# Kernel optimization log

Hardware: AMD Instinct MI355X
Metric: run time of the kernel (lower is better)

Reference implementation:

```python
import jax, jax.numpy as jnp
import numpy as np

NEG_SLOPE = 0.2  # PyG GATConv default


def gat_conv(x, src, dst, W, a_src, a_dst, bias, n):
    # x: [N, Fin] -> h: [N, Fout]
    h = x @ W
    alpha_s = h @ a_src  # [N]
    alpha_d = h @ a_dst  # [N]
    e = jax.nn.leaky_relu(alpha_s[src] + alpha_d[dst], NEG_SLOPE)  # [E]
    # segment softmax over incoming edges of each target node
    m = jax.ops.segment_max(e, dst, num_segments=n)
    e = jnp.exp(e - m[dst])
    denom = jax.ops.segment_sum(e, dst, num_segments=n)
    alpha = e / denom[dst]
    out = jax.ops.segment_sum(alpha[:, None] * h[src], dst, num_segments=n)
    return out + bias


def setup_inputs() -> dict:
    key = jax.random.key(0)
    ks = jax.random.split(key, 10)
    N, E, FIN, HID, FOUT = 100000, 3200000, 128, 32, 64
    x = jax.random.normal(ks[0], (N, FIN), dtype=jnp.float32)
    edge_index = jax.random.randint(ks[1], (2, E), 0, N, dtype=jnp.int64)
    s = 1.0 / np.sqrt(FIN)
    W1 = jax.random.normal(ks[2], (FIN, HID), dtype=jnp.float32) * s
    a1_src = jax.random.normal(ks[3], (HID,), dtype=jnp.float32) * 0.1
    a1_dst = jax.random.normal(ks[4], (HID,), dtype=jnp.float32) * 0.1
    b1 = jnp.zeros((HID,), dtype=jnp.float32)
    W2 = jax.random.normal(ks[5], (HID, FOUT), dtype=jnp.float32) * (1.0 / np.sqrt(HID))
    a2_src = jax.random.normal(ks[6], (FOUT,), dtype=jnp.float32) * 0.1
    a2_dst = jax.random.normal(ks[7], (FOUT,), dtype=jnp.float32) * 0.1
    b2 = jnp.zeros((FOUT,), dtype=jnp.float32)
    return {"x": x, "edge_index": edge_index, "W1": W1, "a1_src": a1_src,
            "a1_dst": a1_dst, "b1": b1, "W2": W2, "a2_src": a2_src,
            "a2_dst": a2_dst, "b2": b2}


def reference(x, edge_index, W1, a1_src, a1_dst, b1, W2, a2_src, a2_dst, b2):
    n = x.shape[0]
    # add self loops (GATConv default add_self_loops=True)
    loop = jnp.arange(n, dtype=edge_index.dtype)
    src = jnp.concatenate([edge_index[0], loop])
    dst = jnp.concatenate([edge_index[1], loop])
    h = gat_conv(x, src, dst, W1, a1_src, a1_dst, b1, n)
    h = jax.nn.relu(h)
    out = gat_conv(h, src, dst, W2, a2_src, a2_dst, b2, n)
    return out
```

## Files before the change

kernel.cpp:

```cpp
#include <hip/hip_runtime.h>
#include <cstdint>
#include <cmath>

#define NEG_SLOPE 0.2f
#define BSH 6
#define BR  64
#define CSH 11
#define EBUF_CAP 8192
#define PCHUNK 8192

__device__ __forceinline__ float leaky(float v) { return v > 0.f ? v : NEG_SLOPE * v; }
__device__ __forceinline__ float uf(unsigned u) { return __uint_as_float(u); }

__device__ __forceinline__ unsigned short f2bf(float f) {
    unsigned u = __float_as_uint(f);
    unsigned r = ((u >> 16) & 1u) + 0x7fffu;
    return (unsigned short)((u + r) >> 16);
}
__device__ __forceinline__ float bflo(unsigned q) { return __uint_as_float(q << 16); }
__device__ __forceinline__ float bfhi(unsigned q) { return __uint_as_float(q & 0xffff0000u); }

template <int FIN, int FOUT, int CPR, int LCPR>
__global__ __launch_bounds__(256, 4) void gemm_rows(
    const float* __restrict__ X, const float* __restrict__ W,
    const float* __restrict__ a_src, const float* __restrict__ a_dst,
    unsigned short* __restrict__ H, float* __restrict__ As, float* __restrict__ Ad,
    float* __restrict__ bmax, int N)
{
    constexpr int ROWS = 256 / CPR;
    constexpr int XST = FIN + 4;
    static_assert((1 << LCPR) == CPR && CPR * 4 == FOUT, "geometry");

    __shared__ float Ws[FIN * FOUT];
    __shared__ float Xs[ROWS * XST];
    __shared__ float wmax[4];

    const int tid = threadIdx.x;
    const int base = blockIdx.x * ROWS;

    for (int i = tid; i < FIN * FOUT / 4; i += 256)
        reinterpret_cast<float4*>(Ws)[i] = reinterpret_cast<const float4*>(W)[i];

    for (int i = tid; i < ROWS * FIN / 4; i += 256) {
        int row = i / (FIN / 4);
        int k4 = (i - row * (FIN / 4)) * 4;
        float4 v = make_float4(0.f, 0.f, 0.f, 0.f);
        if (base + row < N)
            v = *reinterpret_cast<const float4*>(&X[(size_t)(base + row) * FIN + k4]);
        *reinterpret_cast<float4*>(&Xs[row * XST + k4]) = v;
    }
    __syncthreads();

    const int colg = tid & (CPR - 1);
    const int row = tid >> LCPR;
    const int c0 = colg * 4;

    float4 acc = make_float4(0.f, 0.f, 0.f, 0.f);

#pragma unroll 2
    for (int k = 0; k < FIN; k += 4) {
        float4 xv = *reinterpret_cast<const float4*>(&Xs[row * XST + k]);
        float4 w0 = *reinterpret_cast<const float4*>(&Ws[(k + 0) * FOUT + c0]);
        float4 w1 = *reinterpret_cast<const float4*>(&Ws[(k + 1) * FOUT + c0]);
        float4 w2 = *reinterpret_cast<const float4*>(&Ws[(k + 2) * FOUT + c0]);
        float4 w3 = *reinterpret_cast<const float4*>(&Ws[(k + 3) * FOUT + c0]);
        acc.x = fmaf(xv.w, w3.x, fmaf(xv.z, w2.x, fmaf(xv.y, w1.x, fmaf(xv.x, w0.x, acc.x))));
        acc.y = fmaf(xv.w, w3.y, fmaf(xv.z, w2.y, fmaf(xv.y, w1.y, fmaf(xv.x, w0.y, acc.y))));
        acc.z = fmaf(xv.w, w3.z, fmaf(xv.z, w2.z, fmaf(xv.y, w1.z, fmaf(xv.x, w0.z, acc.z))));
        acc.w = fmaf(xv.w, w3.w, fmaf(xv.z, w2.w, fmaf(xv.y, w1.w, fmaf(xv.x, w0.w, acc.w))));
    }

    const int grow = base + row;
    if (grow < N) {
        ushort4 hv;
        hv.x = f2bf(acc.x); hv.y = f2bf(acc.y);
        hv.z = f2bf(acc.z); hv.w = f2bf(acc.w);
        *reinterpret_cast<ushort4*>(&H[(size_t)grow * FOUT + c0]) = hv;
    }

    float4 asv = *reinterpret_cast<const float4*>(&a_src[c0]);
    float4 adv = *reinterpret_cast<const float4*>(&a_dst[c0]);
    float ps = acc.x * asv.x + acc.y * asv.y + acc.z * asv.z + acc.w * asv.w;
    float pd = acc.x * adv.x + acc.y * adv.y + acc.z * adv.z + acc.w * adv.w;
#pragma unroll
    for (int ofs = 1; ofs < CPR; ofs <<= 1) {
        ps += __shfl_xor(ps, ofs);
        pd += __shfl_xor(pd, ofs);
    }
    if (colg == 0 && grow < N) { As[grow] = ps; Ad[grow] = pd; }

    float pm = (grow < N) ? ps : -3.0e38f;
#pragma unroll
    for (int ofs = 1; ofs < 64; ofs <<= 1) pm = fmaxf(pm, __shfl_xor(pm, ofs));
    if ((tid & 63) == 0) wmax[tid >> 6] = pm;
    __syncthreads();
    if (tid == 0)
        bmax[blockIdx.x] = fmaxf(fmaxf(wmax[0], wmax[1]), fmaxf(wmax[2], wmax[3]));
}

__global__ __launch_bounds__(256) void reduce_max_kernel(
    const float* __restrict__ bmax, int nb, float* __restrict__ gmax)
{
    __shared__ float sd[256];
    const int t = threadIdx.x;
    float m = -3.0e38f;
    for (int i = t; i < nb; i += 256) m = fmaxf(m, bmax[i]);
    sd[t] = m; __syncthreads();
    for (int ofs = 128; ofs; ofs >>= 1) {
        if (t < ofs) sd[t] = fmaxf(sd[t], sd[t + ofs]);
        __syncthreads();
    }
    if (t == 0) *gmax = sd[0];
}

__global__ __launch_bounds__(256) void chunk_hist(
    const int* __restrict__ dst, int* __restrict__ fineP, int* __restrict__ pcT,
    int E, int NB, int NC, int NCH)
{
    __shared__ int hc[2048];
    const int t = threadIdx.x;
    for (int i = t; i < 2048; i += 256) hc[i] = 0;
    __syncthreads();
    const int base = blockIdx.x * PCHUNK;
    const int end = (base + PCHUNK < E) ? base + PCHUNK : E;
    for (int e = base + t; e < end; e += 256)
        atomicAdd(&hc[dst[e] >> BSH], 1);
    __syncthreads();
    for (int b = t; b < NB; b += 256)
        fineP[(size_t)blockIdx.x * NB + b] = hc[b];
    if (t < NC) {
        int f0 = t << 5;
        int s = 0;
#pragma unroll
        for (int j = 0; j < 32; ++j) {
            int fb = f0 + j;
            if (fb < NB) s += hc[fb];
        }
        pcT[t * NCH + blockIdx.x] = s;
    }
}

__global__ __launch_bounds__(256) void hist_reduce(
    const int* __restrict__ fineP, int* __restrict__ bhist, int NB, int NCH)
{
    int b = blockIdx.x * 256 + threadIdx.x;
    if (b >= NB) return;
    int s = 0;
    for (int i = blockIdx.y; i < NCH; i += gridDim.y)
        s += fineP[(size_t)i * NB + b];
    atomicAdd(&bhist[b], s);
}

__global__ __launch_bounds__(256) void bucket_scan(
    const int* __restrict__ bhist, int* __restrict__ boff,
    int* __restrict__ ftail, int NB)
{
    __shared__ int sd[256];
    const int t = threadIdx.x;
    const int CH = (NB + 255) >> 8;
    int s = 0;
    for (int j = 0; j < CH; ++j) {
        int idx = t * CH + j;
        s += (idx < NB) ? bhist[idx] : 0;
    }
    sd[t] = s; __syncthreads();
    for (int ofs = 1; ofs < 256; ofs <<= 1) {
        int tmp = (t >= ofs) ? sd[t - ofs] : 0;
        __syncthreads();
        sd[t] += tmp;
        __syncthreads();
    }
    int run = sd[t] - s;
    for (int j = 0; j < CH; ++j) {
        int idx = t * CH + j;
        if (idx < NB) {
            boff[idx] = run;
            ftail[idx * 16] = run;
            run += bhist[idx];
        }
    }
    if (t == 255) boff[NB] = run;
}

__global__ __launch_bounds__(256) void coarse_scan(
    const int* __restrict__ pcT, const int* __restrict__ boff,
    int* __restrict__ co, int NB, int NCH)
{
    __shared__ int sd[256];
    const int c = blockIdx.x;
    const int t = threadIdx.x;
    const int f0 = c << 5;
    const int base = boff[f0 < NB ? f0 : NB];
    int carry = 0;
    for (int start = 0; start < NCH; start += 256) {
        int idx = start + t;
        int v = (idx < NCH) ? pcT[(size_t)c * NCH + idx] : 0;
        sd[t] = v; __syncthreads();
        for (int ofs = 1; ofs < 256; ofs <<= 1) {
            int tmp = (t >= ofs) ? sd[t - ofs] : 0;
            __syncthreads();
            sd[t] += tmp;
            __syncthreads();
        }
        int incl = sd[t];
        int total = sd[255];
        if (idx < NCH) co[(size_t)idx * 64 + c] = base + carry + incl - v;
        carry += total;
        __syncthreads();
    }
}

__global__ __launch_bounds__(256) void coarse_partition(
    const int* __restrict__ src, const int* __restrict__ dst,
    const int* __restrict__ co, int* __restrict__ csrA, int E, int NC)
{
    __shared__ int lcur[64], gpos[64];
    const int t = threadIdx.x;
    if (t < 64) lcur[t] = 0;
    if (t < NC) gpos[t] = co[(size_t)blockIdx.x * 64 + t];
    __syncthreads();
    const int base = blockIdx.x * PCHUNK;
    int bb[32], pp[32];
#pragma unroll
    for (int i = 0; i < 32; ++i) {
        int e = base + i * 256 + t;
        bb[i] = -1;
        if (e < E) {
            int sv = src[e], dv = dst[e];
            bb[i] = dv >> CSH;
            pp[i] = (sv << CSH) | (dv & ((1 << CSH) - 1));
        }
    }
#pragma unroll
    for (int i = 0; i < 32; ++i) {
        if (bb[i] >= 0) {
            int b = bb[i];
            csrA[gpos[b] + atomicAdd(&lcur[b], 1)] = pp[i];
        }
    }
}

__global__ __launch_bounds__(256) void fine_partition(
    const int* __restrict__ csrA, const int* __restrict__ boff,
    int* __restrict__ ftail, int* __restrict__ csrB, int NB)
{
    __shared__ int lhist[32], lcur[32], gpos[32];
    const int b = blockIdx.x;
    const int t = threadIdx.x;
    const int f0 = b << 5;
    const int fe = (f0 + 32 < NB) ? f0 + 32 : NB;
    const int cstart = boff[f0 < NB ? f0 : NB];
    const int cend = boff[fe];
    const int start = cstart + blockIdx.y * PCHUNK;
    if (start >= cend) return;
    const int end = (start + PCHUNK < cend) ? start + PCHUNK : cend;
    if (t < 32) { lhist[t] = 0; lcur[t] = 0; }
    __syncthreads();
    int ff[32], pp[32];
#pragma unroll
    for (int i = 0; i < 32; ++i) {
        int e = start + i * 256 + t;
        ff[i] = -1;
        if (e < end) {
            int v = csrA[e];
            int sv = v >> CSH, dl = v & ((1 << CSH) - 1);
            ff[i] = dl >> BSH;
            pp[i] = (sv << BSH) | (dl & (BR - 1));
            atomicAdd(&lhist[ff[i]], 1);
        }
    }
    __syncthreads();
    if (t < 32 && lhist[t]) gpos[t] = atomicAdd(&ftail[(f0 + t) * 16], lhist[t]);
    __syncthreads();
#pragma unroll
    for (int i = 0; i < 32; ++i) {
        if (ff[i] >= 0) {
            int f = ff[i];
            csrB[gpos[f] + atomicAdd(&lcur[f], 1)] = pp[i];
        }
    }
}

__global__ __launch_bounds__(256) void bucket_build(
    int* __restrict__ csr, const int* __restrict__ boff,
    int* __restrict__ off, int N, int NB)
{
    __shared__ int ebuf[EBUF_CAP];
    __shared__ int lcnt[BR];
    __shared__ int lpref[BR];
    const int bi = blockIdx.x;
    const int t = threadIdx.x;
    const int nb0 = bi << BSH;
    const int p0 = boff[bi];
    const int p1 = boff[bi + 1];
    const int cnt = p1 - p0;

    if (t < BR) lcnt[t] = 0;
    __syncthreads();
    for (int i = t; i < cnt; i += 256) {
        int v = csr[p0 + i];
        if (i < EBUF_CAP) ebuf[i] = v;
        atomicAdd(&lcnt[v & (BR - 1)], 1);
    }
    __syncthreads();
    if (t < BR) {
        int c = lcnt[t];
        int sc = c;
#pragma unroll
        for (int ofs = 1; ofs < BR; ofs <<= 1) {
            int o = __shfl_up(sc, ofs);
            if (t >= ofs) sc += o;
        }
        lpref[t] = sc - c;
        int n = nb0 + t;
        if (n < N) off[n] = p0 + sc - c;
        lcnt[t] = 0;
    }
    if (bi == NB - 1 && t == 0) off[N] = p1;
    __syncthreads();
    for (int i = t; i < cnt && i < EBUF_CAP; i += 256) {
        int v = ebuf[i];
        int ln = v & (BR - 1);
        int p = atomicAdd(&lcnt[ln], 1);
        csr[p0 + lpref[ln] + p] = v >> BSH;
    }
}

template <int F, bool RELU>
__global__ __launch_bounds__(256) void gat_aggregate(
    const int* __restrict__ csr, const int* __restrict__ off,
    const float* __restrict__ As, const float* __restrict__ Ad,
    const unsigned short* __restrict__ Hb, const float* __restrict__ bias,
    const float* __restrict__ gmax, float* __restrict__ Out, int N)
{
    constexpr int LPR = F / 4;
    constexpr int EPI = 64 / LPR;
    constexpr unsigned RB = F * 2;

    __shared__ uint2 pr[4][64];
    const int wave = threadIdx.x >> 6;
    const int lane = threadIdx.x & 63;
    const int n = blockIdx.x * 4 + wave;
    if (n >= N) return;

    const int o0 = off[n];
    const int deg = off[n + 1] - o0;
    const float adn = Ad[n];
    const float eself = leaky(As[n] + adn);
    const float m = leaky(*gmax + adn);

    uint2* myp = pr[wave];
    const char* Hc = (const char*)Hb;
    const int subg = lane / LPR;
    const unsigned f8 = (unsigned)(lane & (LPR - 1)) * 8u;

    float4 acc = make_float4(0.f, 0.f, 0.f, 0.f);
    float denp = 0.f;

    for (int c = 0; c < deg; c += 64) {
        int i = c + lane;
        float w = 0.f; unsigned sb = 0;
        if (i < deg) {
            int s = csr[o0 + i];
            w = __expf(leaky(As[s] + adn) - m);
            sb = (unsigned)s * RB;
            denp += w;
        }
        myp[lane] = make_uint2(sb, __float_as_uint(w));
        int lim = (deg - c < 64) ? deg - c : 64;
        int j = subg;
        for (; j + 3 * EPI < lim; j += 4 * EPI) {
            uint2 p0 = myp[j], p1 = myp[j + EPI], p2 = myp[j + 2 * EPI], p3 = myp[j + 3 * EPI];
            uint2 q0 = *(const uint2*)(Hc + p0.x + f8);
            uint2 q1 = *(const uint2*)(Hc + p1.x + f8);
            uint2 q2 = *(const uint2*)(Hc + p2.x + f8);
            uint2 q3 = *(const uint2*)(Hc + p3.x + f8);
            float w0 = uf(p0.y), w1 = uf(p1.y), w2 = uf(p2.y), w3 = uf(p3.y);
            acc.x = fmaf(w0, bflo(q0.x), acc.x); acc.y = fmaf(w0, bfhi(q0.x), acc.y);
            acc.z = fmaf(w0, bflo(q0.y), acc.z); acc.w = fmaf(w0, bfhi(q0.y), acc.w);
            acc.x = fmaf(w1, bflo(q1.x), acc.x); acc.y = fmaf(w1, bfhi(q1.x), acc.y);
            acc.z = fmaf(w1, bflo(q1.y), acc.z); acc.w = fmaf(w1, bfhi(q1.y), acc.w);
            acc.x = fmaf(w2, bflo(q2.x), acc.x); acc.y = fmaf(w2, bfhi(q2.x), acc.y);
            acc.z = fmaf(w2, bflo(q2.y), acc.z); acc.w = fmaf(w2, bfhi(q2.y), acc.w);
            acc.x = fmaf(w3, bflo(q3.x), acc.x); acc.y = fmaf(w3, bfhi(q3.x), acc.y);
            acc.z = fmaf(w3, bflo(q3.y), acc.z); acc.w = fmaf(w3, bfhi(q3.y), acc.w);
        }
        for (; j < lim; j += EPI) {
            uint2 p = myp[j];
            uint2 q = *(const uint2*)(Hc + p.x + f8);
            float w0 = uf(p.y);
            acc.x = fmaf(w0, bflo(q.x), acc.x); acc.y = fmaf(w0, bfhi(q.x), acc.y);
            acc.z = fmaf(w0, bflo(q.y), acc.z); acc.w = fmaf(w0, bfhi(q.y), acc.w);
        }
    }

#pragma unroll
    for (int ofs = 32; ofs >= LPR; ofs >>= 1) {
        acc.x += __shfl_xor(acc.x, ofs);
        acc.y += __shfl_xor(acc.y, ofs);
        acc.z += __shfl_xor(acc.z, ofs);
        acc.w += __shfl_xor(acc.w, ofs);
    }
#pragma unroll
    for (int ofs = 1; ofs < 64; ofs <<= 1) denp += __shfl_xor(denp, ofs);

    float wsf = __expf(eself - m);
    uint2 qs = *(const uint2*)(Hc + (size_t)n * RB + f8);
    acc.x = fmaf(wsf, bflo(qs.x), acc.x); acc.y = fmaf(wsf, bfhi(qs.x), acc.y);
    acc.z = fmaf(wsf, bflo(qs.y), acc.z); acc.w = fmaf(wsf, bfhi(qs.y), acc.w);
    float den = denp + wsf;

    if (subg == 0) {
        int fi = (lane & (LPR - 1)) * 4;
        float4 bv = *reinterpret_cast<const float4*>(&bias[fi]);
        float4 v;
        v.x = acc.x / den + bv.x;
        v.y = acc.y / den + bv.y;
        v.z = acc.z / den + bv.z;
        v.w = acc.w / den + bv.w;
        if (RELU) {
            v.x = fmaxf(v.x, 0.f); v.y = fmaxf(v.y, 0.f);
            v.z = fmaxf(v.z, 0.f); v.w = fmaxf(v.w, 0.f);
        }
        *reinterpret_cast<float4*>(&Out[(size_t)n * F + fi]) = v;
    }
}

extern "C" void kernel_launch(void* const* d_in, const int* in_sizes, int n_in,
                              void* d_out, int out_size, void* d_ws, size_t ws_size,
                              hipStream_t stream)
{
    const float* x   = (const float*)d_in[0];
    const int*   ei  = (const int*)d_in[1];
    const float* W1  = (const float*)d_in[2];
    const float* a1s = (const float*)d_in[3];
    const float* a1d = (const float*)d_in[4];
    const float* b1  = (const float*)d_in[5];
    const float* W2  = (const float*)d_in[6];
    const float* a2s = (const float*)d_in[7];
    const float* a2d = (const float*)d_in[8];
    const float* b2  = (const float*)d_in[9];

    const int N = in_sizes[0] / 128;
    const int E = in_sizes[1] / 2;
    const int NB = (N + BR - 1) >> BSH;
    const int NC = (N + (1 << CSH) - 1) >> CSH;
    const int NCH = (E + PCHUNK - 1) / PCHUNK;
    const int* src = ei;
    const int* dst = ei + E;
    float* out = (float*)d_out;

    const int g1 = (N + 31) / 32;
    const int g2 = (N + 15) / 16;

    float* ws = (float*)d_ws;
    size_t o = 0;
    unsigned short* h1b = (unsigned short*)(ws + o); o += (size_t)N * 16;
    float* h1a = ws + o; o += (size_t)N * 32;
    unsigned short* h2b = (unsigned short*)(ws + o); o += (size_t)N * 32;
    float* as1 = ws + o; o += N;
    float* ad1 = ws + o; o += N;
    float* as2 = ws + o; o += N;
    float* ad2 = ws + o; o += N;
    float* bmax = ws + o; o += (size_t)g2;
    float* gmax1 = ws + o; o += 1;
    float* gmax2 = ws + o; o += 1;
    int* ip = (int*)(ws + o);
    size_t io = 0;
    int* bhist = ip + io; io += NB;
    int* boff  = ip + io; io += (NB + 1);
    int* ftail = ip + io; io += (size_t)NB * 16;
    int* off   = ip + io; io += (N + 1);
    int* pcT   = ip + io; io += (size_t)NC * NCH;
    int* co    = ip + io; io += (size_t)NCH * 64;
    int* fineP = ip + io; io += (size_t)NCH * NB;
    int* csrA  = ip + io; io += E;
    int* csrB  = ip + io; io += E;

    hipMemsetAsync(bhist, 0, (size_t)NB * sizeof(int), stream);

    chunk_hist<<<NCH, 256, 0, stream>>>(dst, fineP, pcT, E, NB, NC, NCH);
    hist_reduce<<<dim3((NB + 255) / 256, 8), 256, 0, stream>>>(fineP, bhist, NB, NCH);
    bucket_scan<<<1, 256, 0, stream>>>(bhist, boff, ftail, NB);
    coarse_scan<<<NC, 256, 0, stream>>>(pcT, boff, co, NB, NCH);
    coarse_partition<<<NCH, 256, 0, stream>>>(src, dst, co, csrA, E, NC);
    fine_partition<<<dim3(NC, 9), 256, 0, stream>>>(csrA, boff, ftail, csrB, NB);
    bucket_build<<<NB, 256, 0, stream>>>(csrB, boff, off, N, NB);

    const int gn = (N + 3) / 4;

    gemm_rows<128, 32, 8, 3><<<g1, 256, 0, stream>>>(
        x, W1, a1s, a1d, h1b, as1, ad1, bmax, N);
    reduce_max_kernel<<<1, 256, 0, stream>>>(bmax, g1, gmax1);
    gat_aggregate<32, true><<<gn, 256, 0, stream>>>(
        csrB, off, as1, ad1, h1b, b1, gmax1, h1a, N);

    gemm_rows<32, 64, 16, 4><<<g2, 256, 0, stream>>>(
        h1a, W2, a2s, a2d, h2b, as2, ad2, bmax, N);
    reduce_max_kernel<<<1, 256, 0, stream>>>(bmax, g2, gmax2);
    gat_aggregate<64, false><<<gn, 256, 0, stream>>>(
        csrB, off, as2, ad2, h2b, b2, gmax2, out, N);
}
```

Before: 279.7 us.

## Replace three-pass CSR build with two-level 512-node bucket partition and node sort

Restructures the CSR construction from coarse partition (2048-node buckets), fine partition (64-node buckets) and per-bucket build into a single coarse partition into 512-node buckets followed by one node_sort kernel per bucket. That kernel does a local shared-memory histogram, scan and scatter straight from global memory. This drops the fine histogram matrix, hist_reduce, bucket_scan, fine_partition and a full extra pass over E edges. The cost is a wider per-block scatter in coarse_partition (up to 256 buckets with shared atomics) and node_sort reading csrA twice without staging it in shared memory. The loss of locality in the final scatter may also hurt.

```diff
diff --git a/kernel.cpp b/kernel.cpp
--- a/kernel.cpp
+++ b/kernel.cpp
@@ -4,9 +4,9 @@
 
 #define NEG_SLOPE 0.2f
 #define BSH 6
-#define BR  64
-#define CSH 11
-#define EBUF_CAP 8192
+#define CSH 9
+#define CBN 512
+#define RATIO 8
 #define PCHUNK 8192
 
 __device__ __forceinline__ float leaky(float v) { return v > 0.f ? v : NEG_SLOPE * v; }
@@ -114,8 +114,8 @@
 }
 
 __global__ __launch_bounds__(256) void chunk_hist(
-    const int* __restrict__ dst, int* __restrict__ fineP, int* __restrict__ pcT,
-    int E, int NB, int NC, int NCH)
+    const int* __restrict__ dst, int* __restrict__ pcT,
+    int E, int NB, int NCC, int NCH)
 {
     __shared__ int hc[2048];
     const int t = threadIdx.x;
@@ -126,71 +126,59 @@
     for (int e = base + t; e < end; e += 256)
         atomicAdd(&hc[dst[e] >> BSH], 1);
     __syncthreads();
-    for (int b = t; b < NB; b += 256)
-        fineP[(size_t)blockIdx.x * NB + b] = hc[b];
-    if (t < NC) {
-        int f0 = t << 5;
+    if (t < NCC) {
+        int f0 = t * RATIO;
         int s = 0;
 #pragma unroll
-        for (int j = 0; j < 32; ++j) {
+        for (int j = 0; j < RATIO; ++j) {
             int fb = f0 + j;
             if (fb < NB) s += hc[fb];
         }
-        pcT[t * NCH + blockIdx.x] = s;
-    }
-}
-
-__global__ __launch_bounds__(256) void hist_reduce(
-    const int* __restrict__ fineP, int* __restrict__ bhist, int NB, int NCH)
-{
-    int b = blockIdx.x * 256 + threadIdx.x;
-    if (b >= NB) return;
+        pcT[(size_t)t * NCH + blockIdx.x] = s;
+    }
+}
+
+__global__ __launch_bounds__(256) void coarse_total(
+    const int* __restrict__ pcT, int* __restrict__ totals, int NCH)
+{
+    __shared__ int sd[256];
+    const int t = threadIdx.x;
     int s = 0;
-    for (int i = blockIdx.y; i < NCH; i += gridDim.y)
-        s += fineP[(size_t)i * NB + b];
-    atomicAdd(&bhist[b], s);
-}
-
-__global__ __launch_bounds__(256) void bucket_scan(
-    const int* __restrict__ bhist, int* __restrict__ boff,
-    int* __restrict__ ftail, int NB)
+    for (int i = t; i < NCH; i += 256)
+        s += pcT[(size_t)blockIdx.x * NCH + i];
+    sd[t] = s; __syncthreads();
+    for (int ofs = 128; ofs; ofs >>= 1) {
+        if (t < ofs) sd[t] += sd[t + ofs];
+        __syncthreads();
+    }
+    if (t == 0) totals[blockIdx.x] = sd[0];
+}
+
+__global__ __launch_bounds__(256) void boffc_scan(
+    const int* __restrict__ totals, int* __restrict__ boffC, int NCC)
 {
     __shared__ int sd[256];
     const int t = threadIdx.x;
-    const int CH = (NB + 255) >> 8;
-    int s = 0;
-    for (int j = 0; j < CH; ++j) {
-        int idx = t * CH + j;
-        s += (idx < NB) ? bhist[idx] : 0;
-    }
-    sd[t] = s; __syncthreads();
+    int v = (t < NCC) ? totals[t] : 0;
+    sd[t] = v; __syncthreads();
     for (int ofs = 1; ofs < 256; ofs <<= 1) {
         int tmp = (t >= ofs) ? sd[t - ofs] : 0;
         __syncthreads();
         sd[t] += tmp;
         __syncthreads();
     }
-    int run = sd[t] - s;
-    for (int j = 0; j < CH; ++j) {
-        int idx = t * CH + j;
-        if (idx < NB) {
-            boff[idx] = run;
-            ftail[idx * 16] = run;
-            run += bhist[idx];
-        }
-    }
-    if (t == 255) boff[NB] = run;
+    if (t < NCC) boffC[t] = sd[t] - v;
+    if (t == 255) boffC[NCC] = sd[255];
 }
 
 __global__ __launch_bounds__(256) void coarse_scan(
-    const int* __restrict__ pcT, const int* __restrict__ boff,
-    int* __restrict__ co, int NB, int NCH)
+    const int* __restrict__ pcT, const int* __restrict__ boffC,
+    int* __restrict__ co, int NCH)
 {
     __shared__ int sd[256];
     const int c = blockIdx.x;
     const int t = threadIdx.x;
-    const int f0 = c << 5;
-    const int base = boff[f0 < NB ? f0 : NB];
+    const int base = boffC[c];
     int carry = 0;
     for (int start = 0; start < NCH; start += 256) {
         int idx = start + t;
@@ -204,7 +192,7 @@
         }
         int incl = sd[t];
         int total = sd[255];
-        if (idx < NCH) co[(size_t)idx * 64 + c] = base + carry + incl - v;
+        if (idx < NCH) co[(size_t)idx * 256 + c] = base + carry + incl - v;
         carry += total;
         __syncthreads();
     }
@@ -212,12 +200,12 @@
 
 __global__ __launch_bounds__(256) void coarse_partition(
     const int* __restrict__ src, const int* __restrict__ dst,
-    const int* __restrict__ co, int* __restrict__ csrA, int E, int NC)
-{
-    __shared__ int lcur[64], gpos[64];
-    const int t = threadIdx.x;
-    if (t < 64) lcur[t] = 0;
-    if (t < NC) gpos[t] = co[(size_t)blockIdx.x * 64 + t];
+    const int* __restrict__ co, int* __restrict__ csrA, int E, int NCC)
+{
+    __shared__ int lcur[256], gpos[256];
+    const int t = threadIdx.x;
+    lcur[t] = 0;
+    if (t < NCC) gpos[t] = co[(size_t)blockIdx.x * 256 + t];
     __syncthreads();
     const int base = blockIdx.x * PCHUNK;
     int bb[32], pp[32];
@@ -228,7 +216,7 @@
         if (e < E) {
             int sv = src[e], dv = dst[e];
             bb[i] = dv >> CSH;
-            pp[i] = (sv << CSH) | (dv & ((1 << CSH) - 1));
+            pp[i] = (sv << CSH) | (dv & (CBN - 1));
         }
     }
 #pragma unroll
@@ -240,89 +228,48 @@
     }
 }
 
-__global__ __launch_bounds__(256) void fine_partition(
-    const int* __restrict__ csrA, const int* __restrict__ boff,
-    int* __restrict__ ftail, int* __restrict__ csrB, int NB)
-{
-    __shared__ int lhist[32], lcur[32], gpos[32];
-    const int b = blockIdx.x;
-    const int t = threadIdx.x;
-    const int f0 = b << 5;
-    const int fe = (f0 + 32 < NB) ? f0 + 32 : NB;
-    const int cstart = boff[f0 < NB ? f0 : NB];
-    const int cend = boff[fe];
-    const int start = cstart + blockIdx.y * PCHUNK;
-    if (start >= cend) return;
-    const int end = (start + PCHUNK < cend) ? start + PCHUNK : cend;
-    if (t < 32) { lhist[t] = 0; lcur[t] = 0; }
-    __syncthreads();
-    int ff[32], pp[32];
-#pragma unroll
-    for (int i = 0; i < 32; ++i) {
-        int e = start + i * 256 + t;
-        ff[i] = -1;
-        if (e < end) {
-            int v = csrA[e];
-            int sv = v >> CSH, dl = v & ((1 << CSH) - 1);
-            ff[i] = dl >> BSH;
-            pp[i] = (sv << BSH) | (dl & (BR - 1));
-            atomicAdd(&lhist[ff[i]], 1);
-        }
-    }
-    __syncthreads();
-    if (t < 32 && lhist[t]) gpos[t] = atomicAdd(&ftail[(f0 + t) * 16], lhist[t]);
-    __syncthreads();
-#pragma unroll
-    for (int i = 0; i < 32; ++i) {
-        if (ff[i] >= 0) {
-            int f = ff[i];
-            csrB[gpos[f] + atomicAdd(&lcur[f], 1)] = pp[i];
-        }
-    }
-}
-
-__global__ __launch_bounds__(256) void bucket_build(
-    int* __restrict__ csr, const int* __restrict__ boff,
-    int* __restrict__ off, int N, int NB)
-{
-    __shared__ int ebuf[EBUF_CAP];
-    __shared__ int lcnt[BR];
-    __shared__ int lpref[BR];
-    const int bi = blockIdx.x;
-    const int t = threadIdx.x;
-    const int nb0 = bi << BSH;
-    const int p0 = boff[bi];
-    const int p1 = boff[bi + 1];
-    const int cnt = p1 - p0;
-
-    if (t < BR) lcnt[t] = 0;
-    __syncthreads();
-    for (int i = t; i < cnt; i += 256) {
-        int v = csr[p0 + i];
-        if (i < EBUF_CAP) ebuf[i] = v;
-        atomicAdd(&lcnt[v & (BR - 1)], 1);
-    }
-    __syncthreads();
-    if (t < BR) {
-        int c = lcnt[t];
-        int sc = c;
-#pragma unroll
-        for (int ofs = 1; ofs < BR; ofs <<= 1) {
-            int o = __shfl_up(sc, ofs);
-            if (t >= ofs) sc += o;
-        }
-        lpref[t] = sc - c;
-        int n = nb0 + t;
-        if (n < N) off[n] = p0 + sc - c;
-        lcnt[t] = 0;
-    }
-    if (bi == NB - 1 && t == 0) off[N] = p1;
-    __syncthreads();
-    for (int i = t; i < cnt && i < EBUF_CAP; i += 256) {
-        int v = ebuf[i];
-        int ln = v & (BR - 1);
-        int p = atomicAdd(&lcnt[ln], 1);
-        csr[p0 + lpref[ln] + p] = v >> BSH;
+__global__ __launch_bounds__(256) void node_sort(
+    const int* __restrict__ csrA, const int* __restrict__ boffC,
+    int* __restrict__ off, int* __restrict__ csr, int N, int NCC, int E)
+{
+    __shared__ int cnt[CBN];
+    __shared__ int pref[CBN];
+    __shared__ int sd[256];
+    const int c = blockIdx.x;
+    const int t = threadIdx.x;
+    const int p0 = boffC[c];
+    const int p1 = boffC[c + 1];
+    const int n0 = c << CSH;
+
+    for (int i = t; i < CBN; i += 256) cnt[i] = 0;
+    __syncthreads();
+    for (int i = p0 + t; i < p1; i += 256)
+        atomicAdd(&cnt[csrA[i] & (CBN - 1)], 1);
+    __syncthreads();
+    int a0 = cnt[2 * t], a1 = cnt[2 * t + 1];
+    int pairsum = a0 + a1;
+    sd[t] = pairsum; __syncthreads();
+    for (int ofs = 1; ofs < 256; ofs <<= 1) {
+        int tmp = (t >= ofs) ? sd[t - ofs] : 0;
+        __syncthreads();
+        sd[t] += tmp;
+        __syncthreads();
+    }
+    int run = sd[t] - pairsum;
+    pref[2 * t] = run;
+    pref[2 * t + 1] = run + a0;
+    int n = n0 + 2 * t;
+    if (n < N) off[n] = p0 + run;
+    if (n + 1 < N) off[n + 1] = p0 + run + a0;
+    if (c == NCC - 1 && t == 0) off[N] = E;
+    __syncthreads();
+    for (int i = t; i < CBN; i += 256) cnt[i] = 0;
+    __syncthreads();
+    for (int i = p0 + t; i < p1; i += 256) {
+        int v = csrA[i];
+        int ln = v & (CBN - 1);
+        int p = atomicAdd(&cnt[ln], 1);
+        csr[p0 + pref[ln] + p] = v >> CSH;
     }
 }
 
@@ -443,8 +390,8 @@
 
     const int N = in_sizes[0] / 128;
     const int E = in_sizes[1] / 2;
-    const int NB = (N + BR - 1) >> BSH;
-    const int NC = (N + (1 << CSH) - 1) >> CSH;
+    const int NB = (N + 63) >> BSH;
+    const int NCC = (N + CBN - 1) >> CSH;
     const int NCH = (E + PCHUNK - 1) / PCHUNK;
     const int* src = ei;
     const int* dst = ei + E;
@@ -467,25 +414,21 @@
     float* gmax2 = ws + o; o += 1;
     int* ip = (int*)(ws + o);
     size_t io = 0;
-    int* bhist = ip + io; io += NB;
-    int* boff  = ip + io; io += (NB + 1);
-    int* ftail = ip + io; io += (size_t)NB * 16;
-    int* off   = ip + io; io += (N + 1);
-    int* pcT   = ip + io; io += (size_t)NC * NCH;
-    int* co    = ip + io; io += (size_t)NCH * 64;
-    int* fineP = ip + io; io += (size_t)NCH * NB;
-    int* csrA  = ip + io; io += E;
-    int* csrB  = ip + io; io += E;
-
-    hipMemsetAsync(bhist, 0, (size_t)NB * sizeof(int), stream);
-
-    chunk_hist<<<NCH, 256, 0, stream>>>(dst, fineP, pcT, E, NB, NC, NCH);
-    hist_reduce<<<dim3((NB + 255) / 256, 8), 256, 0, stream>>>(fineP, bhist, NB, NCH);
-    bucket_scan<<<1, 256, 0, stream>>>(bhist, boff, ftail, NB);
-    coarse_scan<<<NC, 256, 0, stream>>>(pcT, boff, co, NB, NCH);
-    coarse_partition<<<NCH, 256, 0, stream>>>(src, dst, co, csrA, E, NC);
-    fine_partition<<<dim3(NC, 9), 256, 0, stream>>>(csrA, boff, ftail, csrB, NB);
-    bucket_build<<<NB, 256, 0, stream>>>(csrB, boff, off, N, NB);
+    int* pcT    = ip + io; io += (size_t)NCC * NCH;
+    int* totals = ip + io; io += NCC;
+    int* boffC  = ip + io; io += (NCC + 1);
+    int* co     = ip + io; io += (size_t)NCH * 256;
+    int* off    = ip + io; io += (N + 1);
+    int* csrA   = ip + io; io += E;
+    int* csr    = ip + io; io += E;
+
+
+    chunk_hist<<<NCH, 256, 0, stream>>>(dst, pcT, E, NB, NCC, NCH);
+    coarse_total<<<NCC, 256, 0, stream>>>(pcT, totals, NCH);
+    boffc_scan<<<1, 256, 0, stream>>>(totals, boffC, NCC);
+    coarse_scan<<<NCC, 256, 0, stream>>>(pcT, boffC, co, NCH);
+    coarse_partition<<<NCH, 256, 0, stream>>>(src, dst, co, csrA, E, NCC);
+    node_sort<<<NCC, 256, 0, stream>>>(csrA, boffC, off, csr, N, NCC, E);
 
     const int gn = (N + 3) / 4;
 
@@ -493,11 +436,11 @@
         x, W1, a1s, a1d, h1b, as1, ad1, bmax, N);
     reduce_max_kernel<<<1, 256, 0, stream>>>(bmax, g1, gmax1);
     gat_aggregate<32, true><<<gn, 256, 0, stream>>>(
-        csrB, off, as1, ad1, h1b, b1, gmax1, h1a, N);
+        csr, off, as1, ad1, h1b, b1, gmax1, h1a, N);
 
     gemm_rows<32, 64, 16, 4><<<g2, 256, 0, stream>>>(
         h1a, W2, a2s, a2d, h2b, as2, ad2, bmax, N);
     reduce_max_kernel<<<1, 256, 0, stream>>>(bmax, g2, gmax2);
     gat_aggregate<64, false><<<gn, 256, 0, stream>>>(
-        csrB, off, as2, ad2, h2b, b2, gmax2, out, N);
-}
+        csr, off, as2, ad2, h2b, b2, gmax2, out, N);
+}
```

Result: faster. 265.3 us (-5.2%).
